# Optimization experiments

Hardware: AMD Instinct MI355X
Metric: run time of the kernel (lower is better)

The kernel has to match this reference:

```python
import jax, jax.numpy as jnp
import numpy as np

N_S, N_G, E = 4000, 50000, 250000   # sample nodes, gene nodes, edges per relation
D, H, C1, C3 = 128, 4, 32, 64       # input dim, heads, layer-1 per-head dim, layer-3 per-head dim
NEG_SLOPE = 0.2


def gatv2(x_src, x_dst, src, dst, ea, Wl, bl, Wr, br, We, att, bias, n_dst, concat):
    """PyG GATv2Conv (add_self_loops=False, edge_dim=1, eval mode)."""
    Hh, C = att.shape
    xl = (x_src @ Wl + bl).reshape(-1, Hh, C)          # [N_src, H, C]
    xr = (x_dst @ Wr + br).reshape(-1, Hh, C)          # [N_dst, H, C]
    ee = (ea @ We).reshape(-1, Hh, C)                  # [E, H, C]
    m = jax.nn.leaky_relu(xl[src] + xr[dst] + ee, NEG_SLOPE)   # [E, H, C]
    logits = jnp.einsum('ehc,hc->eh', m, att)          # [E, H]
    # segment softmax over incoming edges of each destination node
    lmax = jax.ops.segment_max(logits, dst, num_segments=n_dst)[dst]
    ex = jnp.exp(logits - lmax)
    denom = jax.ops.segment_sum(ex, dst, num_segments=n_dst)[dst]
    alpha = ex / denom                                 # [E, H]
    out = jax.ops.segment_sum(xl[src] * alpha[:, :, None], dst, num_segments=n_dst)  # [N_dst, H, C]
    out = out.reshape(n_dst, Hh * C) if concat else out.mean(axis=1)
    return out + bias


def setup_inputs() -> dict:
    key = jax.random.key(0)
    ks = jax.random.split(key, 40)
    p = lambda i, shape: jax.random.normal(ks[i], shape, dtype=jnp.float32) * 0.05
    HC1, HC3 = H * C1, H * C3
    inp = {
        'x_mrna': p(0, (N_S, D)),
        'x_gene': p(1, (N_G, D)),
        'sg_src': jax.random.randint(ks[2], (E,), 0, N_S),
        'sg_dst': jax.random.randint(ks[3], (E,), 0, N_G),
        'gs_src': jax.random.randint(ks[4], (E,), 0, N_G),
        'gs_dst': jax.random.randint(ks[5], (E,), 0, N_S),
        'ea_sg': p(6, (E, 1)),
        'ea_gs': p(7, (E, 1)),
        # layer-1 GATv2 params, relation mrna->gene
        'Wl1_sg': p(8, (D, HC1)), 'bl1_sg': p(9, (HC1,)),
        'Wr1_sg': p(10, (D, HC1)), 'br1_sg': p(11, (HC1,)),
        'We1_sg': p(12, (1, HC1)), 'att1_sg': p(13, (H, C1)), 'bo1_sg': p(14, (HC1,)),
        # layer-1 GATv2 params, relation gene->mrna
        'Wl1_gs': p(15, (D, HC1)), 'bl1_gs': p(16, (HC1,)),
        'Wr1_gs': p(17, (D, HC1)), 'br1_gs': p(18, (HC1,)),
        'We1_gs': p(19, (1, HC1)), 'att1_gs': p(20, (H, C1)), 'bo1_gs': p(21, (HC1,)),
        # layer-3 GATv2 params, relation gene->mrna (concat=False)
        'Wl3_gs': p(22, (HC1, HC3)), 'bl3_gs': p(23, (HC3,)),
        'Wr3_gs': p(24, (HC1, HC3)), 'br3_gs': p(25, (HC3,)),
        'We3_gs': p(26, (1, HC3)), 'att3_gs': p(27, (H, C3)), 'bo3_gs': p(28, (C3,)),
        # self-loop linears for omic ('mrna') nodes
        'Wsl1': p(29, (D, C1)), 'bsl1': p(30, (C1,)),
        'Wsl3': p(31, (HC1, C3)), 'bsl3': p(32, (C3,)),
    }
    return inp


def reference(x_mrna, x_gene, sg_src, sg_dst, gs_src, gs_dst, ea_sg, ea_gs,
              Wl1_sg, bl1_sg, Wr1_sg, br1_sg, We1_sg, att1_sg, bo1_sg,
              Wl1_gs, bl1_gs, Wr1_gs, br1_gs, We1_gs, att1_gs, bo1_gs,
              Wl3_gs, bl3_gs, Wr3_gs, br3_gs, We3_gs, att3_gs, bo3_gs,
              Wsl1, bsl1, Wsl3, bsl3):
    # ---- layer 1 (HeteroConv over both relations) ----
    x1_gene = gatv2(x_mrna, x_gene, sg_src, sg_dst, ea_sg,
                    Wl1_sg, bl1_sg, Wr1_sg, br1_sg, We1_sg, att1_sg, bo1_sg, N_G, True)
    x1_mrna = gatv2(x_gene, x_mrna, gs_src, gs_dst, ea_gs,
                    Wl1_gs, bl1_gs, Wr1_gs, br1_gs, We1_gs, att1_gs, bo1_gs, N_S, True)
    # self-loop linear on omic nodes, repeated across heads (repeat(1, heads))
    x1_mrna = x1_mrna + jnp.tile(x_mrna @ Wsl1 + bsl1, (1, H))
    x1_mrna = jax.nn.relu(x1_mrna)
    x1_gene = jax.nn.relu(x1_gene)
    # ---- three_layers=False: x2 = x1; layer 3 (concat=False, head mean) ----
    x3_mrna = gatv2(x1_gene, x1_mrna, gs_src, gs_dst, ea_gs,
                    Wl3_gs, bl3_gs, Wr3_gs, br3_gs, We3_gs, att3_gs, bo3_gs, N_S, False)
    x3_mrna = x3_mrna + (x1_mrna @ Wsl3 + bsl3)
    x3_mrna = jax.nn.relu(x3_mrna)
    # integrator=None, single omic view -> squeeze to [N_S, C3]
    return x3_mrna
```

## Files before the change

kernel.cpp:

```cpp
#include <hip/hip_runtime.h>
#include <cstdint>
#include <cstddef>

#define NS 4000
#define NG 50000
#define NE 250000
#define DIM 128
#define NDST_TOT (NG + NS)

typedef __bf16 bf16_t;
typedef bf16_t bf16x8 __attribute__((ext_vector_type(8)));
typedef bf16_t bf16x4 __attribute__((ext_vector_type(4)));
typedef bf16_t bf16x2 __attribute__((ext_vector_type(2)));
typedef float floatx4 __attribute__((ext_vector_type(4)));

#define HIST_B 245
#define WT_TOT 143360
#define XM_W 64000
#define XG_W 800000
#define PREP_B 3935
struct HPArgs {
  const int* sgd; const int* gsd;
  int* cnt; unsigned short* rank_sg; unsigned short* rank_gs;
  const float* W[8]; bf16_t* Wt[8]; int N[8]; int e0[8];
  const float* xm; bf16_t* xbm;
  const float* xg; bf16_t* xbg;
};

__global__ __launch_bounds__(256) void histprep(HPArgs a) {
  if (blockIdx.x < HIST_B) {
    int e4 = (blockIdx.x * 256 + (int)threadIdx.x) * 4;
    if (e4 < NE) {
      int4 ds = *reinterpret_cast<const int4*>(a.sgd + e4);
      int4 dg = *reinterpret_cast<const int4*>(a.gsd + e4);
      int r0 = atomicAdd(a.cnt + ds.x, 1);
      int r1 = atomicAdd(a.cnt + ds.y, 1);
      int r2 = atomicAdd(a.cnt + ds.z, 1);
      int r3 = atomicAdd(a.cnt + ds.w, 1);
      int g0 = atomicAdd(a.cnt + NG + dg.x, 1);
      int g1 = atomicAdd(a.cnt + NG + dg.y, 1);
      int g2 = atomicAdd(a.cnt + NG + dg.z, 1);
      int g3 = atomicAdd(a.cnt + NG + dg.w, 1);
      ushort4 rs;
      rs.x = (unsigned short)r0; rs.y = (unsigned short)r1;
      rs.z = (unsigned short)r2; rs.w = (unsigned short)r3;
      *reinterpret_cast<ushort4*>(a.rank_sg + e4) = rs;
      ushort4 rg;
      rg.x = (unsigned short)g0; rg.y = (unsigned short)g1;
      rg.z = (unsigned short)g2; rg.w = (unsigned short)g3;
      *reinterpret_cast<ushort4*>(a.rank_gs + e4) = rg;
    }
  } else {
    int u = (blockIdx.x - HIST_B) * 256 + threadIdx.x;
    if (u < WT_TOT) {
      int c = 0;
#pragma unroll
      for (int i = 1; i < 8; i++) if (u >= a.e0[i]) c = i;
      int idx = u - a.e0[c];
      int N = a.N[c];
      int k = idx / N, n = idx - k * N;
      a.Wt[c][n * 128 + k] = (bf16_t)a.W[c][idx];
    } else if (u < WT_TOT + XM_W) {
      int j = (u - WT_TOT) * 8;
      float4 v0 = *reinterpret_cast<const float4*>(a.xm + j);
      float4 v1 = *reinterpret_cast<const float4*>(a.xm + j + 4);
      bf16x8 b;
      b[0] = (bf16_t)v0.x; b[1] = (bf16_t)v0.y; b[2] = (bf16_t)v0.z; b[3] = (bf16_t)v0.w;
      b[4] = (bf16_t)v1.x; b[5] = (bf16_t)v1.y; b[6] = (bf16_t)v1.z; b[7] = (bf16_t)v1.w;
      *reinterpret_cast<bf16x8*>(a.xbm + j) = b;
    } else {
      int j = (u - WT_TOT - XM_W) * 8;
      float4 v0 = *reinterpret_cast<const float4*>(a.xg + j);
      float4 v1 = *reinterpret_cast<const float4*>(a.xg + j + 4);
      bf16x8 b;
      b[0] = (bf16_t)v0.x; b[1] = (bf16_t)v0.y; b[2] = (bf16_t)v0.z; b[3] = (bf16_t)v0.w;
      b[4] = (bf16_t)v1.x; b[5] = (bf16_t)v1.y; b[6] = (bf16_t)v1.z; b[7] = (bf16_t)v1.w;
      *reinterpret_cast<bf16x8*>(a.xbg + j) = b;
    }
  }
}

__global__ __launch_bounds__(1024) void scan1(const int* __restrict__ cnt,
                                              int* __restrict__ rp,
                                              int* __restrict__ csum, int n) {
  __shared__ int wsum[16];
  int i = blockIdx.x * 1024 + threadIdx.x;
  int lane = threadIdx.x & 63, w = threadIdx.x >> 6;
  int v = (i < n) ? cnt[i] : 0;
  int x = v;
#pragma unroll
  for (int off = 1; off < 64; off <<= 1) {
    int y = __shfl_up(x, off);
    if (lane >= off) x += y;
  }
  if (lane == 63) wsum[w] = x;
  __syncthreads();
  if (w == 0 && lane < 16) {
    int s = wsum[lane];
#pragma unroll
    for (int off = 1; off < 16; off <<= 1) {
      int y = __shfl_up(s, off);
      if (lane >= off) s += y;
    }
    wsum[lane] = s;
  }
  __syncthreads();
  int incl = x + (w ? wsum[w - 1] : 0);
  if (i < n) rp[i] = incl - v;
  if (threadIdx.x == 1023) csum[blockIdx.x] = incl;
}

__global__ __launch_bounds__(1024) void scan3(int* __restrict__ rp,
                                              const int* __restrict__ csum, int n) {
  __shared__ int pfx_s;
  if (threadIdx.x < 64) {
    int lane = threadIdx.x;
    int v = (lane < (int)blockIdx.x) ? csum[lane] : 0;
#pragma unroll
    for (int off = 32; off > 0; off >>= 1) v += __shfl_down(v, off);
    if (lane == 0) pfx_s = v;
  }
  __syncthreads();
  int i = blockIdx.x * 1024 + threadIdx.x;
  if (i < n) rp[i] += pfx_s;
  if (i == 0) rp[n] = 2 * NE;
}

#define SCAT_HALF 245
#define SCAT_B 490
struct SGArgs {
  const int* sgd; const int* gsd; const int* sgs; const int* gss;
  const float* easg; const float* eags;
  const int* rp; const unsigned short* rank_sg; const unsigned short* rank_gs;
  uint2* meta;
  const bf16_t* X[5];
  const bf16_t* Wt[5];
  const float* Bv[5];
  bf16_t* Y[5];
  int M[5];
  int Ncol[5];
  int blk0[5];
};

__global__ __launch_bounds__(256, 4) void scatgemm(SGArgs a) {
  if (blockIdx.x < SCAT_B) {
    int rel = (int)blockIdx.x >= SCAT_HALF;
    int b = (int)blockIdx.x - (rel ? SCAT_HALF : 0);
    int t4 = (b * 256 + (int)threadIdx.x) * 4;
    if (t4 < NE) {
      const int* dp = rel ? a.gsd : a.sgd;
      const int* sp = rel ? a.gss : a.sgs;
      const float* ep = rel ? a.eags : a.easg;
      const unsigned short* rk = rel ? a.rank_gs : a.rank_sg;
      const int* rpb = a.rp + (rel ? NG : 0);
      int4 d4 = *reinterpret_cast<const int4*>(dp + t4);
      int4 s4 = *reinterpret_cast<const int4*>(sp + t4);
      float4 e4 = *reinterpret_cast<const float4*>(ep + t4);
      ushort4 r4 = *reinterpret_cast<const ushort4*>(rk + t4);
      int p0 = rpb[d4.x] + (int)r4.x;
      int p1 = rpb[d4.y] + (int)r4.y;
      int p2 = rpb[d4.z] + (int)r4.z;
      int p3 = rpb[d4.w] + (int)r4.w;
      uint2 v0, v1, v2, v3;
      v0.x = (unsigned)s4.x; v0.y = __float_as_uint(e4.x);
      v1.x = (unsigned)s4.y; v1.y = __float_as_uint(e4.y);
      v2.x = (unsigned)s4.z; v2.y = __float_as_uint(e4.z);
      v3.x = (unsigned)s4.w; v3.y = __float_as_uint(e4.w);
      a.meta[p0] = v0;
      a.meta[p1] = v1;
      a.meta[p2] = v2;
      a.meta[p3] = v3;
    }
    return;
  }
  int bid = blockIdx.x - SCAT_B;
  int c = 0;
#pragma unroll
  for (int i = 1; i < 5; i++) if (bid >= a.blk0[i]) c = i;
  const bf16_t* X = a.X[c];
  const bf16_t* Wt = a.Wt[c];
  const float* B = a.Bv[c];
  bf16_t* Y = a.Y[c];
  int M = a.M[c];
  int N = a.Ncol[c];

  int wv = threadIdx.x >> 6, lane = threadIdx.x & 63;
  int m16 = lane & 15, quad = lane >> 4;
  int wrow0 = (bid - a.blk0[c]) * 256 + wv * 64;

  bf16x8 afrag[4][4];
#pragma unroll
  for (int rt = 0; rt < 4; rt++) {
    int arow = wrow0 + rt * 16 + m16;
    const bf16_t* xp = X + (size_t)arow * DIM + quad * 8;
#pragma unroll
    for (int kk = 0; kk < 4; kk++) {
      bf16x8 av = {};
      if (arow < M) av = *reinterpret_cast<const bf16x8*>(xp + kk * 32);
      afrag[rt][kk] = av;
    }
  }

  int ncols = N >> 4;
  for (int nt = 0; nt < ncols; nt++) {
    const bf16_t* bptr = Wt + (size_t)(nt * 16 + m16) * DIM + quad * 8;
    bf16x8 bfrag[4];
#pragma unroll
    for (int kk = 0; kk < 4; kk++)
      bfrag[kk] = *reinterpret_cast<const bf16x8*>(bptr + kk * 32);
    float4 bias = *reinterpret_cast<const float4*>(B + nt * 16 + quad * 4);
#pragma unroll
    for (int rt = 0; rt < 4; rt++) {
      floatx4 acc = {0.f, 0.f, 0.f, 0.f};
#pragma unroll
      for (int kk = 0; kk < 4; kk++)
        acc = __builtin_amdgcn_mfma_f32_16x16x32_bf16(bfrag[kk], afrag[rt][kk], acc, 0, 0, 0);
      int row = wrow0 + rt * 16 + m16;
      if (row < M) {
        bf16x4 o;
        o[0] = (bf16_t)(acc[0] + bias.x);
        o[1] = (bf16_t)(acc[1] + bias.y);
        o[2] = (bf16_t)(acc[2] + bias.z);
        o[3] = (bf16_t)(acc[3] + bias.w);
        *reinterpret_cast<bf16x4*>(Y + (size_t)row * N + nt * 16 + quad * 4) = o;
      }
    }
  }
}

template <int NCFG>
struct GArgs {
  const bf16_t* X[NCFG];
  const bf16_t* Wt[NCFG];
  const float* Bv[NCFG];
  bf16_t* Y[NCFG];
  int M[NCFG];
  int Ncol[NCFG];
  int blk0[NCFG];
};

template <int NCFG>
__global__ __launch_bounds__(256, 4) void gemm_multi(GArgs<NCFG> a) {
  int c = 0;
#pragma unroll
  for (int i = 1; i < NCFG; i++) if ((int)blockIdx.x >= a.blk0[i]) c = i;
  const bf16_t* X = a.X[c];
  const bf16_t* Wt = a.Wt[c];
  const float* B = a.Bv[c];
  bf16_t* Y = a.Y[c];
  int M = a.M[c];
  int N = a.Ncol[c];

  int wv = threadIdx.x >> 6, lane = threadIdx.x & 63;
  int m16 = lane & 15, quad = lane >> 4;
  int wrow0 = ((int)blockIdx.x - a.blk0[c]) * 128 + wv * 32;

  bf16x8 afrag[2][4];
#pragma unroll
  for (int rt = 0; rt < 2; rt++) {
    int arow = wrow0 + rt * 16 + m16;
    const bf16_t* xp = X + (size_t)arow * DIM + quad * 8;
#pragma unroll
    for (int kk = 0; kk < 4; kk++) {
      bf16x8 av = {};
      if (arow < M) av = *reinterpret_cast<const bf16x8*>(xp + kk * 32);
      afrag[rt][kk] = av;
    }
  }

  int ncols = N >> 4;
  for (int nt = 0; nt < ncols; nt++) {
    const bf16_t* bptr = Wt + (size_t)(nt * 16 + m16) * DIM + quad * 8;
    bf16x8 bfrag[4];
#pragma unroll
    for (int kk = 0; kk < 4; kk++)
      bfrag[kk] = *reinterpret_cast<const bf16x8*>(bptr + kk * 32);
    float4 bias = *reinterpret_cast<const float4*>(B + nt * 16 + quad * 4);
#pragma unroll
    for (int rt = 0; rt < 2; rt++) {
      floatx4 acc = {0.f, 0.f, 0.f, 0.f};
#pragma unroll
      for (int kk = 0; kk < 4; kk++)
        acc = __builtin_amdgcn_mfma_f32_16x16x32_bf16(bfrag[kk], afrag[rt][kk], acc, 0, 0, 0);
      int row = wrow0 + rt * 16 + m16;
      if (row < M) {
        bf16x4 o;
        o[0] = (bf16_t)(acc[0] + bias.x);
        o[1] = (bf16_t)(acc[1] + bias.y);
        o[2] = (bf16_t)(acc[2] + bias.z);
        o[3] = (bf16_t)(acc[3] + bias.w);
        *reinterpret_cast<bf16x4*>(Y + (size_t)row * N + nt * 16 + quad * 4) = o;
      }
    }
  }
}

#define EDGE8(cx, eacv)                                                    \
  do {                                                                     \
    float p = 0.f;                                                         \
    _Pragma("unroll")                                                      \
    for (int v = 0; v < 8; v++) {                                          \
      float z = fmaf(eacv, wev[v], xrv[v]) + (float)cx[v];                 \
      z = z > 0.f ? z : 0.2f * z;                                          \
      p = fmaf(z, atv[v], p);                                              \
    }                                                                      \
    p += __shfl_xor(p, 1);                                                 \
    p += __shfl_xor(p, 2);                                                 \
    float ex = __expf(p);                                                  \
    den += ex;                                                             \
    _Pragma("unroll")                                                      \
    for (int v = 0; v < 8; v++) acc[v] = fmaf(ex, (float)cx[v], acc[v]);   \
  } while (0)

#define SGB 3125
__global__ __launch_bounds__(256) void gatC(
    const int* __restrict__ rp, const uint2* __restrict__ meta,
    const float* __restrict__ WeS, const float* __restrict__ attS,
    const float* __restrict__ boS,
    const bf16_t* __restrict__ xlS, const bf16_t* __restrict__ xrS,
    bf16_t* __restrict__ outS,
    const float* __restrict__ WeG, const float* __restrict__ attG,
    const float* __restrict__ boG,
    const bf16_t* __restrict__ xlG, const bf16_t* __restrict__ xrG,
    const bf16_t* __restrict__ slG, bf16_t* __restrict__ outG) {
  __shared__ uint2 smeta[256];
  __shared__ float lacc[16][128];
  __shared__ float lden[16][4];
  int lane = threadIdx.x & 63, wv = threadIdx.x >> 6;
  int gl = lane & 15, grp = lane >> 4;

  if (blockIdx.x < SGB) {
    int wid = blockIdx.x * 4 + wv;
    int d0 = wid * 4;
    int q = lane < 5 ? lane : 0;
    int rv = rp[d0 + q];
    int beg = __shfl(rv, grp), end = __shfl(rv, grp + 1);
    int dst = d0 + grp;

    float wev[8], atv[8], xrv[8], acc[8];
    *reinterpret_cast<float4*>(wev) = *reinterpret_cast<const float4*>(WeS + gl * 8);
    *reinterpret_cast<float4*>(wev + 4) = *reinterpret_cast<const float4*>(WeS + gl * 8 + 4);
    *reinterpret_cast<float4*>(atv) = *reinterpret_cast<const float4*>(attS + gl * 8);
    *reinterpret_cast<float4*>(atv + 4) = *reinterpret_cast<const float4*>(attS + gl * 8 + 4);
    bf16x8 xrb = *reinterpret_cast<const bf16x8*>(xrS + (size_t)dst * 128 + gl * 8);
#pragma unroll
    for (int v = 0; v < 8; v++) { xrv[v] = (float)xrb[v]; acc[v] = 0.f; }
    float den = 0.f;

    for (int i0 = beg; i0 < end; i0 += 16) {
      int cnt = min(16, end - i0);
      int s_l = 0; float ea_l = 0.f;
      if (gl < cnt) {
        uint2 mv = meta[i0 + gl];
        s_l = (int)mv.x; ea_l = __uint_as_float(mv.y);
      }
      int base = lane & 48;
      float eaA = __shfl(ea_l, base);
      bf16x8 xA = *reinterpret_cast<const bf16x8*>(
          xlS + (size_t)__shfl(s_l, base) * 128 + gl * 8);
      float eaB = 0.f; bf16x8 xB = {};
      if (cnt > 1) {
        eaB = __shfl(ea_l, base + 1);
        xB = *reinterpret_cast<const bf16x8*>(
            xlS + (size_t)__shfl(s_l, base + 1) * 128 + gl * 8);
      }
      for (int k = 0; k < cnt; k++) {
        bf16x8 cur = xA;
        float eac = eaA;
        eaA = eaB; xA = xB;
        if (k + 2 < cnt) {
          eaB = __shfl(ea_l, base + k + 2);
          xB = *reinterpret_cast<const bf16x8*>(
              xlS + (size_t)__shfl(s_l, base + k + 2) * 128 + gl * 8);
        }
        EDGE8(cur, eac);
      }
    }
    float inv = den > 0.f ? 1.f / den : 0.f;
    bf16x8 o;
#pragma unroll
    for (int v = 0; v < 8; v++) {
      float val = acc[v] * inv + boS[gl * 8 + v];
      o[v] = (bf16_t)(val > 0.f ? val : 0.f);
    }
    *reinterpret_cast<bf16x8*>(outS + (size_t)dst * 128 + gl * 8) = o;
  } else {
    int d = (int)blockIdx.x - SGB;
    const int* rpg = rp + NG;
    int G = wv * 4 + grp;
    int tid = threadIdx.x;

    float wev[8], atv[8], xrv[8], acc[8];
    *reinterpret_cast<float4*>(wev) = *reinterpret_cast<const float4*>(WeG + gl * 8);
    *reinterpret_cast<float4*>(wev + 4) = *reinterpret_cast<const float4*>(WeG + gl * 8 + 4);
    *reinterpret_cast<float4*>(atv) = *reinterpret_cast<const float4*>(attG + gl * 8);
    *reinterpret_cast<float4*>(atv + 4) = *reinterpret_cast<const float4*>(attG + gl * 8 + 4);
    bf16x8 xrb = *reinterpret_cast<const bf16x8*>(xrG + (size_t)d * 128 + gl * 8);
#pragma unroll
    for (int v = 0; v < 8; v++) { xrv[v] = (float)xrb[v]; acc[v] = 0.f; }
    float den = 0.f;

    int beg = rpg[d], end = rpg[d + 1];
    for (int base = beg; base < end; base += 256) {
      int cntb = min(256, end - base);
      __syncthreads();
      if (tid < cntb) smeta[tid] = meta[base + tid];
      __syncthreads();
      uint2 mvA = {}, mvB = {};
      bf16x8 xA = {}, xB = {};
      if (G < cntb) {
        mvA = smeta[G];
        xA = *reinterpret_cast<const bf16x8*>(xlG + (size_t)mvA.x * 128 + gl * 8);
      }
      if (G + 16 < cntb) {
        mvB = smeta[G + 16];
        xB = *reinterpret_cast<const bf16x8*>(xlG + (size_t)mvB.x * 128 + gl * 8);
      }
      for (int e = G; e < cntb; e += 32) {
        float eacA = __uint_as_float(mvA.y);
        bf16x8 cA = xA;
        if (e + 32 < cntb) {
          mvA = smeta[e + 32];
          xA = *reinterpret_cast<const bf16x8*>(xlG + (size_t)mvA.x * 128 + gl * 8);
        }
        EDGE8(cA, eacA);
        if (e + 16 < cntb) {
          float eacB = __uint_as_float(mvB.y);
          bf16x8 cB = xB;
          if (e + 48 < cntb) {
            mvB = smeta[e + 48];
            xB = *reinterpret_cast<const bf16x8*>(xlG + (size_t)mvB.x * 128 + gl * 8);
          }
          EDGE8(cB, eacB);
        }
      }
    }
#pragma unroll
    for (int v = 0; v < 8; v++) lacc[G][gl * 8 + v] = acc[v];
    if ((gl & 3) == 0) lden[G][gl >> 2] = den;
    __syncthreads();
    if (wv != 0) return;
    int ch = lane * 2;
    int h = lane >> 4;
    float a0 = 0.f, a1 = 0.f, dh = 0.f;
#pragma unroll
    for (int g2 = 0; g2 < 16; g2++) {
      a0 += lacc[g2][ch];
      a1 += lacc[g2][ch + 1];
      dh += lden[g2][h];
    }
    float inv = dh > 0.f ? 1.f / dh : 0.f;
    float v0 = a0 * inv + boG[ch] + (float)slG[(size_t)d * 32 + (ch & 31)];
    float v1 = a1 * inv + boG[ch + 1] + (float)slG[(size_t)d * 32 + ((ch + 1) & 31)];
    bf16x2 o;
    o[0] = (bf16_t)(v0 > 0.f ? v0 : 0.f);
    o[1] = (bf16_t)(v1 > 0.f ? v1 : 0.f);
    *reinterpret_cast<bf16x2*>(outG + (size_t)d * 128 + ch) = o;
  }
}

#define EDGE16(c0, c1, eacv)                                                  \
  do {                                                                        \
    float p = 0.f;                                                            \
    _Pragma("unroll")                                                         \
    for (int v = 0; v < 8; v++) {                                             \
      float z = fmaf(eacv, wev[v], xrv[v]) + (float)c0[v];                    \
      z = z > 0.f ? z : 0.2f * z;                                             \
      p = fmaf(z, atv[v], p);                                                 \
    }                                                                         \
    _Pragma("unroll")                                                         \
    for (int v = 0; v < 8; v++) {                                             \
      float z = fmaf(eacv, wev[v + 8], xrv[v + 8]) + (float)c1[v];            \
      z = z > 0.f ? z : 0.2f * z;                                             \
      p = fmaf(z, atv[v + 8], p);                                             \
    }                                                                         \
    p += __shfl_xor(p, 1);                                                    \
    p += __shfl_xor(p, 2);                                                    \
    float ex = __expf(p);                                                     \
    den += ex;                                                                \
    _Pragma("unroll")                                                         \
    for (int v = 0; v < 8; v++) acc[v] = fmaf(ex, (float)c0[v], acc[v]);      \
    _Pragma("unroll")                                                         \
    for (int v = 0; v < 8; v++) acc[v + 8] = fmaf(ex, (float)c1[v], acc[v + 8]); \
  } while (0)

__global__ __launch_bounds__(256) void gatE(
    const int* __restrict__ rp, const uint2* __restrict__ meta,
    const float* __restrict__ We, const float* __restrict__ att,
    const bf16_t* __restrict__ xl, const bf16_t* __restrict__ xr,
    const float* __restrict__ bo, const bf16_t* __restrict__ sl,
    float* __restrict__ out) {
  __shared__ uint2 smeta[256];
  __shared__ float lacc[16][256];
  __shared__ float lden[16][4];
  int lane = threadIdx.x & 63, wv = threadIdx.x >> 6;
  int gl = lane & 15, grp = lane >> 4;
  int G = wv * 4 + grp;
  int tid = threadIdx.x;
  int d = blockIdx.x;

  float wev[16], atv[16], xrv[16], acc[16];
#pragma unroll
  for (int b = 0; b < 4; b++) {
    *reinterpret_cast<float4*>(wev + b * 4) =
        *reinterpret_cast<const float4*>(We + gl * 16 + b * 4);
    *reinterpret_cast<float4*>(atv + b * 4) =
        *reinterpret_cast<const float4*>(att + gl * 16 + b * 4);
  }
  {
    bf16x8 r0 = *reinterpret_cast<const bf16x8*>(xr + (size_t)d * 256 + gl * 16);
    bf16x8 r1 = *reinterpret_cast<const bf16x8*>(xr + (size_t)d * 256 + gl * 16 + 8);
#pragma unroll
    for (int v = 0; v < 8; v++) { xrv[v] = (float)r0[v]; xrv[v + 8] = (float)r1[v]; }
  }
#pragma unroll
  for (int v = 0; v < 16; v++) acc[v] = 0.f;
  float den = 0.f;

  int beg = rp[d], end = rp[d + 1];
  for (int base = beg; base < end; base += 256) {
    int cntb = min(256, end - base);
    __syncthreads();
    if (tid < cntb) smeta[tid] = meta[base + tid];
    __syncthreads();
    uint2 mvA = {}, mvB = {};
    bf16x8 a0 = {}, a1 = {}, b0 = {}, b1 = {};
    if (G < cntb) {
      mvA = smeta[G];
      a0 = *reinterpret_cast<const bf16x8*>(xl + (size_t)mvA.x * 256 + gl * 16);
      a1 = *reinterpret_cast<const bf16x8*>(xl + (size_t)mvA.x * 256 + gl * 16 + 8);
    }
    if (G + 16 < cntb) {
      mvB = smeta[G + 16];
      b0 = *reinterpret_cast<const bf16x8*>(xl + (size_t)mvB.x * 256 + gl * 16);
      b1 = *reinterpret_cast<const bf16x8*>(xl + (size_t)mvB.x * 256 + gl * 16 + 8);
    }
    for (int e = G; e < cntb; e += 32) {
      float eacA = __uint_as_float(mvA.y);
      bf16x8 cA0 = a0, cA1 = a1;
      if (e + 32 < cntb) {
        mvA = smeta[e + 32];
        a0 = *reinterpret_cast<const bf16x8*>(xl + (size_t)mvA.x * 256 + gl * 16);
        a1 = *reinterpret_cast<const bf16x8*>(xl + (size_t)mvA.x * 256 + gl * 16 + 8);
      }
      EDGE16(cA0, cA1, eacA);
      if (e + 16 < cntb) {
        float eacB = __uint_as_float(mvB.y);
        bf16x8 cB0 = b0, cB1 = b1;
        if (e + 48 < cntb) {
          mvB = smeta[e + 48];
          b0 = *reinterpret_cast<const bf16x8*>(xl + (size_t)mvB.x * 256 + gl * 16);
          b1 = *reinterpret_cast<const bf16x8*>(xl + (size_t)mvB.x * 256 + gl * 16 + 8);
        }
        EDGE16(cB0, cB1, eacB);
      }
    }
  }
#pragma unroll
  for (int v = 0; v < 16; v++) lacc[G][gl * 16 + v] = acc[v];
  if ((gl & 3) == 0) lden[G][gl >> 2] = den;
  __syncthreads();
  if (wv != 0) return;
  int ch = lane * 4;
  int h = lane >> 4;
  float a[4] = {0.f, 0.f, 0.f, 0.f};
  float dh = 0.f;
#pragma unroll
  for (int g2 = 0; g2 < 16; g2++) {
#pragma unroll
    for (int v = 0; v < 4; v++) a[v] += lacc[g2][ch + v];
    dh += lden[g2][h];
  }
  float inv = dh > 0.f ? 1.f / dh : 0.f;
#pragma unroll
  for (int v = 0; v < 4; v++) {
    float s_ = a[v] * inv;
    s_ += __shfl_xor(s_, 16);
    s_ += __shfl_xor(s_, 32);
    if (lane < 16) {
      int c = (lane & 15) * 4 + v;
      float val = 0.25f * s_ + bo[c] + (float)sl[(size_t)d * 64 + c];
      out[(size_t)d * 64 + c] = val > 0.f ? val : 0.f;
    }
  }
}


static inline int nblk(long long threads) { return (int)((threads + 255) / 256); }
static inline int nrow(int M, int R) { return (M + R - 1) / R; }

extern "C" void kernel_launch(void* const* d_in, const int* in_sizes, int n_in,
                              void* d_out, int out_size, void* d_ws, size_t ws_size,
                              hipStream_t stream) {
  const float* x_mrna = (const float*)d_in[0];
  const float* x_gene = (const float*)d_in[1];
  const int* sg_src = (const int*)d_in[2];
  const int* sg_dst = (const int*)d_in[3];
  const int* gs_src = (const int*)d_in[4];
  const int* gs_dst = (const int*)d_in[5];
  const float* ea_sg = (const float*)d_in[6];
  const float* ea_gs = (const float*)d_in[7];
  const float* Wl1_sg = (const float*)d_in[8];
  const float* bl1_sg = (const float*)d_in[9];
  const float* Wr1_sg = (const float*)d_in[10];
  const float* br1_sg = (const float*)d_in[11];
  const float* We1_sg = (const float*)d_in[12];
  const float* att1_sg = (const float*)d_in[13];
  const float* bo1_sg = (const float*)d_in[14];
  const float* Wl1_gs = (const float*)d_in[15];
  const float* bl1_gs = (const float*)d_in[16];
  const float* Wr1_gs = (const float*)d_in[17];
  const float* br1_gs = (const float*)d_in[18];
  const float* We1_gs = (const float*)d_in[19];
  const float* att1_gs = (const float*)d_in[20];
  const float* bo1_gs = (const float*)d_in[21];
  const float* Wl3_gs = (const float*)d_in[22];
  const float* bl3_gs = (const float*)d_in[23];
  const float* Wr3_gs = (const float*)d_in[24];
  const float* br3_gs = (const float*)d_in[25];
  const float* We3_gs = (const float*)d_in[26];
  const float* att3_gs = (const float*)d_in[27];
  const float* bo3_gs = (const float*)d_in[28];
  const float* Wsl1 = (const float*)d_in[29];
  const float* bsl1 = (const float*)d_in[30];
  const float* Wsl3 = (const float*)d_in[31];
  const float* bsl3 = (const float*)d_in[32];

  float* ws = (float*)d_ws;
  bf16_t* xl1_gs = (bf16_t*)(ws + 0);
  bf16_t* xl1_sg = (bf16_t*)(ws + 3200000);
  bf16_t* xr1_sg = (bf16_t*)(ws + 3456000);
  bf16_t* xr1_gs = (bf16_t*)(ws + 6656000);
  bf16_t* xl3    = (bf16_t*)(ws + 0);
  bf16_t* xr3    = (bf16_t*)(ws + 6400000);
  bf16_t* xb_mrna = (bf16_t*)(ws + 6912000);
  bf16_t* xb_gene = (bf16_t*)(ws + 7168000);
  bf16_t* x1_gene = (bf16_t*)(ws + 10368000);
  bf16_t* x1_mrna = (bf16_t*)(ws + 13568000);
  bf16_t* sl1    = (bf16_t*)(ws + 13824000);
  bf16_t* sl3    = (bf16_t*)(ws + 13856000);
  int*   ib      = (int*)(ws + 13920000);
  int* cnt  = ib + 0;
  int* rpc  = ib + 54000;
  int* csum = ib + 108002;
  unsigned short* rank_sg = (unsigned short*)(ib + 108066);
  unsigned short* rank_gs = (unsigned short*)(ib + 233066);
  uint2* meta = (uint2*)(ib + 358066);
  bf16_t* wtb = (bf16_t*)(ib + 1358066);

  bf16_t* wt_l1sg = wtb + 0;
  bf16_t* wt_r1sg = wtb + 16384;
  bf16_t* wt_l1gs = wtb + 32768;
  bf16_t* wt_r1gs = wtb + 49152;
  bf16_t* wt_l3   = wtb + 65536;
  bf16_t* wt_r3   = wtb + 98304;
  bf16_t* wt_sl1  = wtb + 131072;
  bf16_t* wt_sl3  = wtb + 135168;

  hipMemsetAsync(cnt, 0, 54000 * sizeof(int), stream);

  {
    HPArgs hp;
    hp.sgd = sg_dst; hp.gsd = gs_dst;
    hp.cnt = cnt; hp.rank_sg = rank_sg; hp.rank_gs = rank_gs;
    const float* Wsrc[8] = {Wl1_sg, Wr1_sg, Wl1_gs, Wr1_gs, Wl3_gs, Wr3_gs, Wsl1, Wsl3};
    bf16_t* Wdst[8] = {wt_l1sg, wt_r1sg, wt_l1gs, wt_r1gs, wt_l3, wt_r3, wt_sl1, wt_sl3};
    int Nn[8] = {128, 128, 128, 128, 256, 256, 32, 64};
    int e0[8] = {0, 16384, 32768, 49152, 65536, 98304, 131072, 135168};
    for (int i = 0; i < 8; i++) { hp.W[i] = Wsrc[i]; hp.Wt[i] = Wdst[i]; hp.N[i] = Nn[i]; hp.e0[i] = e0[i]; }
    hp.xm = x_mrna; hp.xbm = xb_mrna;
    hp.xg = x_gene; hp.xbg = xb_gene;
    histprep<<<HIST_B + PREP_B, 256, 0, stream>>>(hp);
  }

  int nchunks = (NDST_TOT + 1023) / 1024;
  scan1<<<nchunks, 1024, 0, stream>>>(cnt, rpc, csum, NDST_TOT);
  scan3<<<nchunks, 1024, 0, stream>>>(rpc, csum, NDST_TOT);

  {
    SGArgs sa;
    sa.sgd = sg_dst; sa.gsd = gs_dst; sa.sgs = sg_src; sa.gss = gs_src;
    sa.easg = ea_sg; sa.eags = ea_gs;
    sa.rp = rpc; sa.rank_sg = rank_sg; sa.rank_gs = rank_gs; sa.meta = meta;
    const bf16_t* Xs[5] = {xb_mrna, xb_gene, xb_gene, xb_mrna, xb_mrna};
    const bf16_t* Ws[5] = {wt_l1sg, wt_r1sg, wt_l1gs, wt_r1gs, wt_sl1};
    const float* Bs[5] = {bl1_sg, br1_sg, bl1_gs, br1_gs, bsl1};
    bf16_t* Ys[5] = {xl1_sg, xr1_sg, xl1_gs, xr1_gs, sl1};
    int Ms[5] = {NS, NG, NG, NS, NS};
    int Ns[5] = {128, 128, 128, 128, 32};
    int b0 = 0;
    for (int i = 0; i < 5; i++) {
      sa.X[i] = Xs[i]; sa.Wt[i] = Ws[i]; sa.Bv[i] = Bs[i]; sa.Y[i] = Ys[i];
      sa.M[i] = Ms[i]; sa.Ncol[i] = Ns[i]; sa.blk0[i] = b0;
      b0 += nrow(Ms[i], 256);
    }
    scatgemm<<<SCAT_B + b0, 256, 0, stream>>>(sa);
  }

  gatC<<<SGB + NS, 256, 0, stream>>>(
      rpc, meta,
      We1_sg, att1_sg, bo1_sg, xl1_sg, xr1_sg, x1_gene,
      We1_gs, att1_gs, bo1_gs, xl1_gs, xr1_gs, sl1, x1_mrna);

  {
    GArgs<3> ga;
    const bf16_t* Xs[3] = {x1_gene, x1_mrna, x1_mrna};
    const bf16_t* Ws[3] = {wt_l3, wt_r3, wt_sl3};
    const float* Bs[3] = {bl3_gs, br3_gs, bsl3};
    bf16_t* Ys[3] = {xl3, xr3, sl3};
    int Ms[3] = {NG, NS, NS};
    int Ns[3] = {256, 256, 64};
    int b0 = 0;
    for (int i = 0; i < 3; i++) {
      ga.X[i] = Xs[i]; ga.Wt[i] = Ws[i]; ga.Bv[i] = Bs[i]; ga.Y[i] = Ys[i];
      ga.M[i] = Ms[i]; ga.Ncol[i] = Ns[i]; ga.blk0[i] = b0;
      b0 += nrow(Ms[i], 128);
    }
    gemm_multi<3><<<b0, 256, 0, stream>>>(ga);
  }

  gatE<<<NS, 256, 0, stream>>>(rpc + NG, meta, We3_gs, att3_gs,
                               xl3, xr3, bo3_gs, sl3, (float*)d_out);
}
```

Measured before the change: 287.9 us.

## Map one wavefront per sample node in gather kernels, drop LDS reduction

The gene→sample aggregation in gatC and the layer-3 gatE kernel now assign one wavefront per destination sample node instead of one 256-thread block. Edge metadata is read straight from global memory and partial sums are combined with cross-lane shuffles instead of shared-memory staging, __syncthreads and a final LDS reduction. The sample→gene path shortens its prefetch from two edges to one, and the histogram stage goes back to one edge per thread with scalar atomics. This cuts block count and barrier overhead, but each wave now walks about 62 edges serially with less latency hiding per node.

Measured after the change: 290.8 us. About the same (+1.0%).

```diff
diff --git a/kernel.cpp b/kernel.cpp
--- a/kernel.cpp
+++ b/kernel.cpp
@@ -14,7 +14,7 @@
 typedef bf16_t bf16x2 __attribute__((ext_vector_type(2)));
 typedef float floatx4 __attribute__((ext_vector_type(4)));
 
-#define HIST_B 245
+#define HIST_B 977
 #define WT_TOT 143360
 #define XM_W 64000
 #define XG_W 800000
@@ -29,26 +29,10 @@
 
 __global__ __launch_bounds__(256) void histprep(HPArgs a) {
   if (blockIdx.x < HIST_B) {
-    int e4 = (blockIdx.x * 256 + (int)threadIdx.x) * 4;
-    if (e4 < NE) {
-      int4 ds = *reinterpret_cast<const int4*>(a.sgd + e4);
-      int4 dg = *reinterpret_cast<const int4*>(a.gsd + e4);
-      int r0 = atomicAdd(a.cnt + ds.x, 1);
-      int r1 = atomicAdd(a.cnt + ds.y, 1);
-      int r2 = atomicAdd(a.cnt + ds.z, 1);
-      int r3 = atomicAdd(a.cnt + ds.w, 1);
-      int g0 = atomicAdd(a.cnt + NG + dg.x, 1);
-      int g1 = atomicAdd(a.cnt + NG + dg.y, 1);
-      int g2 = atomicAdd(a.cnt + NG + dg.z, 1);
-      int g3 = atomicAdd(a.cnt + NG + dg.w, 1);
-      ushort4 rs;
-      rs.x = (unsigned short)r0; rs.y = (unsigned short)r1;
-      rs.z = (unsigned short)r2; rs.w = (unsigned short)r3;
-      *reinterpret_cast<ushort4*>(a.rank_sg + e4) = rs;
-      ushort4 rg;
-      rg.x = (unsigned short)g0; rg.y = (unsigned short)g1;
-      rg.z = (unsigned short)g2; rg.w = (unsigned short)g3;
-      *reinterpret_cast<ushort4*>(a.rank_gs + e4) = rg;
+    int e = blockIdx.x * 256 + threadIdx.x;
+    if (e < NE) {
+      a.rank_sg[e] = (unsigned short)atomicAdd(a.cnt + a.sgd[e], 1);
+      a.rank_gs[e] = (unsigned short)atomicAdd(a.cnt + NG + a.gsd[e], 1);
     }
   } else {
     int u = (blockIdx.x - HIST_B) * 256 + threadIdx.x;
@@ -312,153 +296,6 @@
     for (int v = 0; v < 8; v++) acc[v] = fmaf(ex, (float)cx[v], acc[v]);   \
   } while (0)
 
-#define SGB 3125
-__global__ __launch_bounds__(256) void gatC(
-    const int* __restrict__ rp, const uint2* __restrict__ meta,
-    const float* __restrict__ WeS, const float* __restrict__ attS,
-    const float* __restrict__ boS,
-    const bf16_t* __restrict__ xlS, const bf16_t* __restrict__ xrS,
-    bf16_t* __restrict__ outS,
-    const float* __restrict__ WeG, const float* __restrict__ attG,
-    const float* __restrict__ boG,
-    const bf16_t* __restrict__ xlG, const bf16_t* __restrict__ xrG,
-    const bf16_t* __restrict__ slG, bf16_t* __restrict__ outG) {
-  __shared__ uint2 smeta[256];
-  __shared__ float lacc[16][128];
-  __shared__ float lden[16][4];
-  int lane = threadIdx.x & 63, wv = threadIdx.x >> 6;
-  int gl = lane & 15, grp = lane >> 4;
-
-  if (blockIdx.x < SGB) {
-    int wid = blockIdx.x * 4 + wv;
-    int d0 = wid * 4;
-    int q = lane < 5 ? lane : 0;
-    int rv = rp[d0 + q];
-    int beg = __shfl(rv, grp), end = __shfl(rv, grp + 1);
-    int dst = d0 + grp;
-
-    float wev[8], atv[8], xrv[8], acc[8];
-    *reinterpret_cast<float4*>(wev) = *reinterpret_cast<const float4*>(WeS + gl * 8);
-    *reinterpret_cast<float4*>(wev + 4) = *reinterpret_cast<const float4*>(WeS + gl * 8 + 4);
-    *reinterpret_cast<float4*>(atv) = *reinterpret_cast<const float4*>(attS + gl * 8);
-    *reinterpret_cast<float4*>(atv + 4) = *reinterpret_cast<const float4*>(attS + gl * 8 + 4);
-    bf16x8 xrb = *reinterpret_cast<const bf16x8*>(xrS + (size_t)dst * 128 + gl * 8);
-#pragma unroll
-    for (int v = 0; v < 8; v++) { xrv[v] = (float)xrb[v]; acc[v] = 0.f; }
-    float den = 0.f;
-
-    for (int i0 = beg; i0 < end; i0 += 16) {
-      int cnt = min(16, end - i0);
-      int s_l = 0; float ea_l = 0.f;
-      if (gl < cnt) {
-        uint2 mv = meta[i0 + gl];
-        s_l = (int)mv.x; ea_l = __uint_as_float(mv.y);
-      }
-      int base = lane & 48;
-      float eaA = __shfl(ea_l, base);
-      bf16x8 xA = *reinterpret_cast<const bf16x8*>(
-          xlS + (size_t)__shfl(s_l, base) * 128 + gl * 8);
-      float eaB = 0.f; bf16x8 xB = {};
-      if (cnt > 1) {
-        eaB = __shfl(ea_l, base + 1);
-        xB = *reinterpret_cast<const bf16x8*>(
-            xlS + (size_t)__shfl(s_l, base + 1) * 128 + gl * 8);
-      }
-      for (int k = 0; k < cnt; k++) {
-        bf16x8 cur = xA;
-        float eac = eaA;
-        eaA = eaB; xA = xB;
-        if (k + 2 < cnt) {
-          eaB = __shfl(ea_l, base + k + 2);
-          xB = *reinterpret_cast<const bf16x8*>(
-              xlS + (size_t)__shfl(s_l, base + k + 2) * 128 + gl * 8);
-        }
-        EDGE8(cur, eac);
-      }
-    }
-    float inv = den > 0.f ? 1.f / den : 0.f;
-    bf16x8 o;
-#pragma unroll
-    for (int v = 0; v < 8; v++) {
-      float val = acc[v] * inv + boS[gl * 8 + v];
-      o[v] = (bf16_t)(val > 0.f ? val : 0.f);
-    }
-    *reinterpret_cast<bf16x8*>(outS + (size_t)dst * 128 + gl * 8) = o;
-  } else {
-    int d = (int)blockIdx.x - SGB;
-    const int* rpg = rp + NG;
-    int G = wv * 4 + grp;
-    int tid = threadIdx.x;
-
-    float wev[8], atv[8], xrv[8], acc[8];
-    *reinterpret_cast<float4*>(wev) = *reinterpret_cast<const float4*>(WeG + gl * 8);
-    *reinterpret_cast<float4*>(wev + 4) = *reinterpret_cast<const float4*>(WeG + gl * 8 + 4);
-    *reinterpret_cast<float4*>(atv) = *reinterpret_cast<const float4*>(attG + gl * 8);
-    *reinterpret_cast<float4*>(atv + 4) = *reinterpret_cast<const float4*>(attG + gl * 8 + 4);
-    bf16x8 xrb = *reinterpret_cast<const bf16x8*>(xrG + (size_t)d * 128 + gl * 8);
-#pragma unroll
-    for (int v = 0; v < 8; v++) { xrv[v] = (float)xrb[v]; acc[v] = 0.f; }
-    float den = 0.f;
-
-    int beg = rpg[d], end = rpg[d + 1];
-    for (int base = beg; base < end; base += 256) {
-      int cntb = min(256, end - base);
-      __syncthreads();
-      if (tid < cntb) smeta[tid] = meta[base + tid];
-      __syncthreads();
-      uint2 mvA = {}, mvB = {};
-      bf16x8 xA = {}, xB = {};
-      if (G < cntb) {
-        mvA = smeta[G];
-        xA = *reinterpret_cast<const bf16x8*>(xlG + (size_t)mvA.x * 128 + gl * 8);
-      }
-      if (G + 16 < cntb) {
-        mvB = smeta[G + 16];
-        xB = *reinterpret_cast<const bf16x8*>(xlG + (size_t)mvB.x * 128 + gl * 8);
-      }
-      for (int e = G; e < cntb; e += 32) {
-        float eacA = __uint_as_float(mvA.y);
-        bf16x8 cA = xA;
-        if (e + 32 < cntb) {
-          mvA = smeta[e + 32];
-          xA = *reinterpret_cast<const bf16x8*>(xlG + (size_t)mvA.x * 128 + gl * 8);
-        }
-        EDGE8(cA, eacA);
-        if (e + 16 < cntb) {
-          float eacB = __uint_as_float(mvB.y);
-          bf16x8 cB = xB;
-          if (e + 48 < cntb) {
-            mvB = smeta[e + 48];
-            xB = *reinterpret_cast<const bf16x8*>(xlG + (size_t)mvB.x * 128 + gl * 8);
-          }
-          EDGE8(cB, eacB);
-        }
-      }
-    }
-#pragma unroll
-    for (int v = 0; v < 8; v++) lacc[G][gl * 8 + v] = acc[v];
-    if ((gl & 3) == 0) lden[G][gl >> 2] = den;
-    __syncthreads();
-    if (wv != 0) return;
-    int ch = lane * 2;
-    int h = lane >> 4;
-    float a0 = 0.f, a1 = 0.f, dh = 0.f;
-#pragma unroll
-    for (int g2 = 0; g2 < 16; g2++) {
-      a0 += lacc[g2][ch];
-      a1 += lacc[g2][ch + 1];
-      dh += lden[g2][h];
-    }
-    float inv = dh > 0.f ? 1.f / dh : 0.f;
-    float v0 = a0 * inv + boG[ch] + (float)slG[(size_t)d * 32 + (ch & 31)];
-    float v1 = a1 * inv + boG[ch + 1] + (float)slG[(size_t)d * 32 + ((ch + 1) & 31)];
-    bf16x2 o;
-    o[0] = (bf16_t)(v0 > 0.f ? v0 : 0.f);
-    o[1] = (bf16_t)(v1 > 0.f ? v1 : 0.f);
-    *reinterpret_cast<bf16x2*>(outG + (size_t)d * 128 + ch) = o;
-  }
-}
-
 #define EDGE16(c0, c1, eacv)                                                  \
   do {                                                                        \
     float p = 0.f;                                                            \
@@ -484,20 +321,141 @@
     for (int v = 0; v < 8; v++) acc[v + 8] = fmaf(ex, (float)c1[v], acc[v + 8]); \
   } while (0)
 
+#define SGB 3125
+#define GS_B 1000
+__global__ __launch_bounds__(256) void gatC(
+    const int* __restrict__ rp, const uint2* __restrict__ meta,
+    const float* __restrict__ WeS, const float* __restrict__ attS,
+    const float* __restrict__ boS,
+    const bf16_t* __restrict__ xlS, const bf16_t* __restrict__ xrS,
+    bf16_t* __restrict__ outS,
+    const float* __restrict__ WeG, const float* __restrict__ attG,
+    const float* __restrict__ boG,
+    const bf16_t* __restrict__ xlG, const bf16_t* __restrict__ xrG,
+    const bf16_t* __restrict__ slG, bf16_t* __restrict__ outG) {
+  int lane = threadIdx.x & 63, wv = threadIdx.x >> 6;
+  int gl = lane & 15, grp = lane >> 4;
+
+  if (blockIdx.x < SGB) {
+    int wid = blockIdx.x * 4 + wv;
+    int d0 = wid * 4;
+    int q = lane < 5 ? lane : 0;
+    int rv = rp[d0 + q];
+    int beg = __shfl(rv, grp), end = __shfl(rv, grp + 1);
+    int dst = d0 + grp;
+
+    float wev[8], atv[8], xrv[8], acc[8];
+    *reinterpret_cast<float4*>(wev) = *reinterpret_cast<const float4*>(WeS + gl * 8);
+    *reinterpret_cast<float4*>(wev + 4) = *reinterpret_cast<const float4*>(WeS + gl * 8 + 4);
+    *reinterpret_cast<float4*>(atv) = *reinterpret_cast<const float4*>(attS + gl * 8);
+    *reinterpret_cast<float4*>(atv + 4) = *reinterpret_cast<const float4*>(attS + gl * 8 + 4);
+    bf16x8 xrb = *reinterpret_cast<const bf16x8*>(xrS + (size_t)dst * 128 + gl * 8);
+#pragma unroll
+    for (int v = 0; v < 8; v++) { xrv[v] = (float)xrb[v]; acc[v] = 0.f; }
+    float den = 0.f;
+
+    for (int i0 = beg; i0 < end; i0 += 16) {
+      int cnt = min(16, end - i0);
+      int s_l = 0; float ea_l = 0.f;
+      if (gl < cnt) {
+        uint2 mv = meta[i0 + gl];
+        s_l = (int)mv.x; ea_l = __uint_as_float(mv.y);
+      }
+      int base = lane & 48;
+      float ea = __shfl(ea_l, base);
+      bf16x8 xlb = *reinterpret_cast<const bf16x8*>(
+          xlS + (size_t)__shfl(s_l, base) * 128 + gl * 8);
+      for (int k = 0; k < cnt; k++) {
+        bf16x8 cur = xlb;
+        float eac = ea;
+        if (k + 1 < cnt) {
+          ea = __shfl(ea_l, base + k + 1);
+          xlb = *reinterpret_cast<const bf16x8*>(
+              xlS + (size_t)__shfl(s_l, base + k + 1) * 128 + gl * 8);
+        }
+        EDGE8(cur, eac);
+      }
+    }
+    float inv = den > 0.f ? 1.f / den : 0.f;
+    bf16x8 o;
+#pragma unroll
+    for (int v = 0; v < 8; v++) {
+      float val = acc[v] * inv + boS[gl * 8 + v];
+      o[v] = (bf16_t)(val > 0.f ? val : 0.f);
+    }
+    *reinterpret_cast<bf16x8*>(outS + (size_t)dst * 128 + gl * 8) = o;
+  } else {
+    int d = ((int)blockIdx.x - SGB) * 4 + wv;
+    const int* rpg = rp + NG;
+    int beg = rpg[d], end = rpg[d + 1];
+
+    float wev[8], atv[8], xrv[8], acc[8];
+    *reinterpret_cast<float4*>(wev) = *reinterpret_cast<const float4*>(WeG + gl * 8);
+    *reinterpret_cast<float4*>(wev + 4) = *reinterpret_cast<const float4*>(WeG + gl * 8 + 4);
+    *reinterpret_cast<float4*>(atv) = *reinterpret_cast<const float4*>(attG + gl * 8);
+    *reinterpret_cast<float4*>(atv + 4) = *reinterpret_cast<const float4*>(attG + gl * 8 + 4);
+    bf16x8 xrb = *reinterpret_cast<const bf16x8*>(xrG + (size_t)d * 128 + gl * 8);
+#pragma unroll
+    for (int v = 0; v < 8; v++) { xrv[v] = (float)xrb[v]; acc[v] = 0.f; }
+    float den = 0.f;
+
+    int e = beg + grp;
+    uint2 mvA = {}, mvB = {};
+    bf16x8 xA = {}, xB = {};
+    if (e < end) mvA = meta[e];
+    if (e + 4 < end) mvB = meta[e + 4];
+    if (e < end)
+      xA = *reinterpret_cast<const bf16x8*>(xlG + (size_t)mvA.x * 128 + gl * 8);
+    if (e + 4 < end)
+      xB = *reinterpret_cast<const bf16x8*>(xlG + (size_t)mvB.x * 128 + gl * 8);
+    for (; e < end; e += 8) {
+      float eacA = __uint_as_float(mvA.y);
+      bf16x8 cA = xA;
+      if (e + 8 < end) {
+        mvA = meta[e + 8];
+        xA = *reinterpret_cast<const bf16x8*>(xlG + (size_t)mvA.x * 128 + gl * 8);
+      }
+      EDGE8(cA, eacA);
+      if (e + 4 < end) {
+        float eacB = __uint_as_float(mvB.y);
+        bf16x8 cB = xB;
+        if (e + 12 < end) {
+          mvB = meta[e + 12];
+          xB = *reinterpret_cast<const bf16x8*>(xlG + (size_t)mvB.x * 128 + gl * 8);
+        }
+        EDGE8(cB, eacB);
+      }
+    }
+#pragma unroll
+    for (int v = 0; v < 8; v++) {
+      acc[v] += __shfl_xor(acc[v], 16);
+      acc[v] += __shfl_xor(acc[v], 32);
+    }
+    den += __shfl_xor(den, 16);
+    den += __shfl_xor(den, 32);
+    if (grp == 0) {
+      float inv = den > 0.f ? 1.f / den : 0.f;
+      int ch = gl * 8;
+      bf16x8 o;
+#pragma unroll
+      for (int v = 0; v < 8; v++) {
+        float val = acc[v] * inv + boG[ch + v] + (float)slG[(size_t)d * 32 + ((ch + v) & 31)];
+        o[v] = (bf16_t)(val > 0.f ? val : 0.f);
+      }
+      *reinterpret_cast<bf16x8*>(outG + (size_t)d * 128 + ch) = o;
+    }
+  }
+}
+
 __global__ __launch_bounds__(256) void gatE(
     const int* __restrict__ rp, const uint2* __restrict__ meta,
     const float* __restrict__ We, const float* __restrict__ att,
     const bf16_t* __restrict__ xl, const bf16_t* __restrict__ xr,
     const float* __restrict__ bo, const bf16_t* __restrict__ sl,
     float* __restrict__ out) {
-  __shared__ uint2 smeta[256];
-  __shared__ float lacc[16][256];
-  __shared__ float lden[16][4];
   int lane = threadIdx.x & 63, wv = threadIdx.x >> 6;
   int gl = lane & 15, grp = lane >> 4;
-  int G = wv * 4 + grp;
-  int tid = threadIdx.x;
-  int d = blockIdx.x;
+  int d = blockIdx.x * 4 + wv;
 
   float wev[16], atv[16], xrv[16], acc[16];
 #pragma unroll
@@ -518,69 +476,72 @@
   float den = 0.f;
 
   int beg = rp[d], end = rp[d + 1];
-  for (int base = beg; base < end; base += 256) {
-    int cntb = min(256, end - base);
-    __syncthreads();
-    if (tid < cntb) smeta[tid] = meta[base + tid];
-    __syncthreads();
-    uint2 mvA = {}, mvB = {};
-    bf16x8 a0 = {}, a1 = {}, b0 = {}, b1 = {};
-    if (G < cntb) {
-      mvA = smeta[G];
+  int e = beg + grp;
+  uint2 mvA = {}, mvB = {};
+  bf16x8 a0 = {}, a1 = {}, b0 = {}, b1 = {};
+  if (e < end) mvA = meta[e];
+  if (e + 4 < end) mvB = meta[e + 4];
+  if (e < end) {
+    a0 = *reinterpret_cast<const bf16x8*>(xl + (size_t)mvA.x * 256 + gl * 16);
+    a1 = *reinterpret_cast<const bf16x8*>(xl + (size_t)mvA.x * 256 + gl * 16 + 8);
+  }
+  if (e + 4 < end) {
+    b0 = *reinterpret_cast<const bf16x8*>(xl + (size_t)mvB.x * 256 + gl * 16);
+    b1 = *reinterpret_cast<const bf16x8*>(xl + (size_t)mvB.x * 256 + gl * 16 + 8);
+  }
+  for (; e < end; e += 8) {
+    float eacA = __uint_as_float(mvA.y);
+    bf16x8 cA0 = a0, cA1 = a1;
+    if (e + 8 < end) {
+      mvA = meta[e + 8];
       a0 = *reinterpret_cast<const bf16x8*>(xl + (size_t)mvA.x * 256 + gl * 16);
       a1 = *reinterpret_cast<const bf16x8*>(xl + (size_t)mvA.x * 256 + gl * 16 + 8);
     }
-    if (G + 16 < cntb) {
-      mvB = smeta[G + 16];
-      b0 = *reinterpret_cast<const bf16x8*>(xl + (size_t)mvB.x * 256 + gl * 16);
-      b1 = *reinterpret_cast<const bf16x8*>(xl + (size_t)mvB.x * 256 + gl * 16 + 8);
-    }
-    for (int e = G; e < cntb; e += 32) {
-      float eacA = __uint_as_float(mvA.y);
-      bf16x8 cA0 = a0, cA1 = a1;
-      if (e + 32 < cntb) {
-        mvA = smeta[e + 32];
-        a0 = *reinterpret_cast<const bf16x8*>(xl + (size_t)mvA.x * 256 + gl * 16);
-        a1 = *reinterpret_cast<const bf16x8*>(xl + (size_t)mvA.x * 256 + gl * 16 + 8);
-      }
-      EDGE16(cA0, cA1, eacA);
-      if (e + 16 < cntb) {
-        float eacB = __uint_as_float(mvB.y);
-        bf16x8 cB0 = b0, cB1 = b1;
-        if (e + 48 < cntb) {
-          mvB = smeta[e + 48];
-          b0 = *reinterpret_cast<const bf16x8*>(xl + (size_t)mvB.x * 256 + gl * 16);
-          b1 = *reinterpret_cast<const bf16x8*>(xl + (size_t)mvB.x * 256 + gl * 16 + 8);
-        }
-        EDGE16(cB0, cB1, eacB);
-      }
-    }
-  }
-#pragma unroll
-  for (int v = 0; v < 16; v++) lacc[G][gl * 16 + v] = acc[v];
-  if ((gl & 3) == 0) lden[G][gl >> 2] = den;
-  __syncthreads();
-  if (wv != 0) return;
-  int ch = lane * 4;
-  int h = lane >> 4;
-  float a[4] = {0.f, 0.f, 0.f, 0.f};
-  float dh = 0.f;
-#pragma unroll
-  for (int g2 = 0; g2 < 16; g2++) {
-#pragma unroll
-    for (int v = 0; v < 4; v++) a[v] += lacc[g2][ch + v];
-    dh += lden[g2][h];
-  }
-  float inv = dh > 0.f ? 1.f / dh : 0.f;
-#pragma unroll
-  for (int v = 0; v < 4; v++) {
-    float s_ = a[v] * inv;
-    s_ += __shfl_xor(s_, 16);
-    s_ += __shfl_xor(s_, 32);
-    if (lane < 16) {
-      int c = (lane & 15) * 4 + v;
-      float val = 0.25f * s_ + bo[c] + (float)sl[(size_t)d * 64 + c];
-      out[(size_t)d * 64 + c] = val > 0.f ? val : 0.f;
+    EDGE16(cA0, cA1, eacA);
+    if (e + 4 < end) {
+      float eacB = __uint_as_float(mvB.y);
+      bf16x8 cB0 = b0, cB1 = b1;
+      if (e + 12 < end) {
+        mvB = meta[e + 12];
+        b0 = *reinterpret_cast<const bf16x8*>(xl + (size_t)mvB.x * 256 + gl * 16);
+        b1 = *reinterpret_cast<const bf16x8*>(xl + (size_t)mvB.x * 256 + gl * 16 + 8);
+      }
+      EDGE16(cB0, cB1, eacB);
+    }
+  }
+
+#pragma unroll
+  for (int v = 0; v < 16; v++) {
+    acc[v] += __shfl_xor(acc[v], 16);
+    acc[v] += __shfl_xor(acc[v], 32);
+  }
+  den += __shfl_xor(den, 16);
+  den += __shfl_xor(den, 32);
+
+  float inv = den > 0.f ? 1.f / den : 0.f;
+  float outv[16];
+#pragma unroll
+  for (int v = 0; v < 16; v++) {
+    float s_ = acc[v] * inv;
+    s_ += __shfl_xor(s_, 4);
+    s_ += __shfl_xor(s_, 8);
+    outv[v] = s_;
+  }
+  if (lane < 4) {
+    int c0 = gl * 16;
+#pragma unroll
+    for (int b = 0; b < 4; b++) {
+      float4 o;
+      float val;
+      val = 0.25f * outv[b * 4 + 0] + bo[c0 + b * 4 + 0] + (float)sl[(size_t)d * 64 + c0 + b * 4 + 0];
+      o.x = val > 0.f ? val : 0.f;
+      val = 0.25f * outv[b * 4 + 1] + bo[c0 + b * 4 + 1] + (float)sl[(size_t)d * 64 + c0 + b * 4 + 1];
+      o.y = val > 0.f ? val : 0.f;
+      val = 0.25f * outv[b * 4 + 2] + bo[c0 + b * 4 + 2] + (float)sl[(size_t)d * 64 + c0 + b * 4 + 2];
+      o.z = val > 0.f ? val : 0.f;
+      val = 0.25f * outv[b * 4 + 3] + bo[c0 + b * 4 + 3] + (float)sl[(size_t)d * 64 + c0 + b * 4 + 3];
+      o.w = val > 0.f ? val : 0.f;
+      *reinterpret_cast<float4*>(out + (size_t)d * 64 + c0 + b * 4) = o;
     }
   }
 }
@@ -697,7 +658,7 @@
     scatgemm<<<SCAT_B + b0, 256, 0, stream>>>(sa);
   }
 
-  gatC<<<SGB + NS, 256, 0, stream>>>(
+  gatC<<<SGB + GS_B, 256, 0, stream>>>(
       rpc, meta,
       We1_sg, att1_sg, bo1_sg, xl1_sg, xr1_sg, x1_gene,
       We1_gs, att1_gs, bo1_gs, xl1_gs, xr1_gs, sl1, x1_mrna);
@@ -719,6 +680,6 @@
     gemm_multi<3><<<b0, 256, 0, stream>>>(ga);
   }
 
-  gatE<<<NS, 256, 0, stream>>>(rpc + NG, meta, We3_gs, att3_gs,
-                               xl3, xr3, bo3_gs, sl3, (float*)d_out);
-}
+  gatE<<<GS_B, 256, 0, stream>>>(rpc + NG, meta, We3_gs, att3_gs,
+                                 xl3, xr3, bo3_gs, sl3, (float*)d_out);
+}
```
